# Performance work log

Measured on AMD Instinct MI355X. Metric: run time of the kernel, lower is better.

The kernel has to match this reference:

```python
import jax, jax.numpy as jnp
import numpy as np

N = 100000          # nodes per node type (paper, author)
E = 250000          # edges per relation
D_IN = 128          # input feature dim
H, C = 4, 32        # heads, channels per head (h_dim = H*C = 128)
HD = H * C
OUT = 349           # num classes
RELS = ["c", "w", "wb"]  # cites(paper->paper), writes(author->paper), written_by(paper->author)


def setup_inputs() -> dict:
    key = jax.random.key(0)
    ks = iter(jax.random.split(key, 64))
    def nrm(shape, scale=0.1):
        return jax.random.normal(next(ks), shape, jnp.float32) * scale
    inp = {
        "x_paper": jax.random.normal(next(ks), (N, D_IN), jnp.float32),
        "x_author": jax.random.normal(next(ks), (N, D_IN), jnp.float32),
        "ei_cites": jax.random.randint(next(ks), (2, E), 0, N),
        "ei_writes": jax.random.randint(next(ks), (2, E), 0, N),
        "ei_written": jax.random.randint(next(ks), (2, E), 0, N),
    }
    for l, din in [(0, D_IN), (1, HD)]:
        for r in RELS:
            inp[f"W{l}_{r}"] = nrm((din, HD))
            inp[f"as{l}_{r}"] = nrm((H, C))
            inp[f"ad{l}_{r}"] = nrm((H, C))
            inp[f"b{l}_{r}"] = jnp.zeros((HD,), jnp.float32)
    inp["lin_W"] = nrm((HD, OUT))
    inp["lin_b"] = jnp.zeros((OUT,), jnp.float32)
    return inp


def _gat_conv(x_src, x_dst, ei, W, att_s, att_d, b, n_dst):
    """PyG GATConv (concat heads, add_self_loops=False, shared lin for src/dst)."""
    h_s = (x_src @ W).reshape(-1, H, C)              # [Ns,H,C]
    h_d = (x_dst @ W).reshape(-1, H, C)              # [Nd,H,C]
    a_s = (h_s * att_s).sum(-1)                      # [Ns,H]
    a_d = (h_d * att_d).sum(-1)                      # [Nd,H]
    src, dst = ei[0], ei[1]
    e = jax.nn.leaky_relu(a_s[src] + a_d[dst], 0.2)  # [E,H]
    # segment softmax over incoming edges per dst node
    m = jax.ops.segment_max(e, dst, num_segments=n_dst)
    m = jnp.where(jnp.isfinite(m), m, 0.0)
    w = jnp.exp(e - m[dst])
    z = jax.ops.segment_sum(w, dst, num_segments=n_dst)
    alpha = w / (z[dst] + 1e-16)                     # [E,H]
    msg = h_s[src] * alpha[..., None]                # [E,H,C]
    agg = jax.ops.segment_sum(msg, dst, num_segments=n_dst)
    return agg.reshape(n_dst, HD) + b


def _forward(x_paper, x_author, ei_cites, ei_writes, ei_written, params, lin_W, lin_b):
    xp, xa = x_paper, x_author
    for l in range(2):
        p = params[l]
        # HeteroConv with sum aggregation across relations per dst node type
        op = _gat_conv(xp, xp, ei_cites, *p["c"], N) + _gat_conv(xa, xp, ei_writes, *p["w"], N)
        oa = _gat_conv(xp, xa, ei_written, *p["wb"], N)
        xp, xa = op, oa
        if l != 1:
            xp = jax.nn.leaky_relu(xp, 0.01)  # F.leaky_relu default slope
            xa = jax.nn.leaky_relu(xa, 0.01)
            # dropout: identity in eval/reference mode
    return xp @ lin_W + lin_b  # [N, OUT]


def reference(x_paper, x_author,
              W0_c, as0_c, ad0_c, b0_c, W0_w, as0_w, ad0_w, b0_w, W0_wb, as0_wb, ad0_wb, b0_wb,
              W1_c, as1_c, ad1_c, b1_c, W1_w, as1_w, ad1_w, b1_w, W1_wb, as1_wb, ad1_wb, b1_wb,
              lin_W, lin_b, ei_cites, ei_writes, ei_written):
    params = [
        {"c": (W0_c, as0_c, ad0_c, b0_c), "w": (W0_w, as0_w, ad0_w, b0_w), "wb": (W0_wb, as0_wb, ad0_wb, b0_wb)},
        {"c": (W1_c, as1_c, ad1_c, b1_c), "w": (W1_w, as1_w, ad1_w, b1_w), "wb": (W1_wb, as1_wb, ad1_wb, b1_wb)},
    ]
    return _forward(x_paper, x_author, ei_cites, ei_writes, ei_written, params, lin_W, lin_b)
```

## Files before the change

kernel.cpp:

```cpp
#include <hip/hip_runtime.h>

#define NN 100000
#define EE 250000
#define CAP 32

typedef unsigned int u32;

__global__ __launch_bounds__(256) void gemm_att(
    const float* __restrict__ X, const float* __restrict__ W,
    const float* __restrict__ atts, const float* __restrict__ attd,
    float* __restrict__ H, float* __restrict__ aS, float* __restrict__ aD)
{
    __shared__ float sW[64 * 128];
    __shared__ float sXT[128 * 32];
    const int tid = threadIdx.x;
    const size_t r0 = (size_t)blockIdx.x * 32;

    {
        int rl = tid & 31, kg = tid >> 5;
        const float4* Xr = (const float4*)(X + (r0 + rl) * 128);
#pragma unroll
        for (int t = 0; t < 4; ++t) {
            float4 u = Xr[kg * 4 + t];
            int k = kg * 16 + t * 4;
            sXT[(k + 0) * 32 + rl] = u.x;
            sXT[(k + 1) * 32 + rl] = u.y;
            sXT[(k + 2) * 32 + rl] = u.z;
            sXT[(k + 3) * 32 + rl] = u.w;
        }
    }

    const int jg = tid & 31;
    const int rg = tid >> 5;
    float acc[4][4] = {};

    for (int kh = 0; kh < 2; ++kh) {
        __syncthreads();
        const float4* Wu = (const float4*)(W + kh * 64 * 128);
        float4* sWv = (float4*)sW;
#pragma unroll
        for (int t = 0; t < 8; ++t)
            sWv[tid + 256 * t] = Wu[tid + 256 * t];
        __syncthreads();
#pragma unroll 4
        for (int k = 0; k < 64; ++k) {
            const float4 w = ((const float4*)sW)[k * 32 + jg];
            const int kk = kh * 64 + k;
            const float4 x = ((const float4*)sXT)[kk * 8 + rg];
            acc[0][0] += w.x * x.x; acc[0][1] += w.y * x.x; acc[0][2] += w.z * x.x; acc[0][3] += w.w * x.x;
            acc[1][0] += w.x * x.y; acc[1][1] += w.y * x.y; acc[1][2] += w.z * x.y; acc[1][3] += w.w * x.y;
            acc[2][0] += w.x * x.z; acc[2][1] += w.y * x.z; acc[2][2] += w.z * x.z; acc[2][3] += w.w * x.z;
            acc[3][0] += w.x * x.w; acc[3][1] += w.y * x.w; acc[3][2] += w.z * x.w; acc[3][3] += w.w * x.w;
        }
    }

    const float4 sv = ((const float4*)atts)[jg];
    const float4 dv = ((const float4*)attd)[jg];
    const int h = jg >> 3;

#pragma unroll
    for (int i = 0; i < 4; ++i) {
        const size_t row = r0 + rg * 4 + i;
        if (H)
            ((float4*)H)[row * 32 + jg] = make_float4(acc[i][0], acc[i][1], acc[i][2], acc[i][3]);
        float ps = acc[i][0] * sv.x + acc[i][1] * sv.y + acc[i][2] * sv.z + acc[i][3] * sv.w;
        float pd = acc[i][0] * dv.x + acc[i][1] * dv.y + acc[i][2] * dv.z + acc[i][3] * dv.w;
        ps += __shfl_xor(ps, 1); ps += __shfl_xor(ps, 2); ps += __shfl_xor(ps, 4);
        pd += __shfl_xor(pd, 1); pd += __shfl_xor(pd, 2); pd += __shfl_xor(pd, 4);
        if ((jg & 7) == 0) {
            aS[row * 4 + h] = ps;
            aD[row * 4 + h] = pd;
        }
    }
}

__global__ __launch_bounds__(256) void fold_w3(
    const float* __restrict__ W0, const float* __restrict__ a0,
    const float* __restrict__ W1, const float* __restrict__ a1,
    const float* __restrict__ W2, const float* __restrict__ a2,
    float* __restrict__ Wf)
{
    int i = blockIdx.x * 256 + threadIdx.x;
    if (i >= 1536) return;
    int r = i >> 9, j = i & 511;
    int k = j >> 2, h = j & 3;
    const float* W = (r == 0) ? W0 : (r == 1) ? W1 : W2;
    const float* a = (r == 0) ? a0 : (r == 1) ? a1 : a2;
    float s = 0.f;
#pragma unroll
    for (int c = 0; c < 32; ++c)
        s += W[k * 128 + h * 32 + c] * a[h * 32 + c];
    Wf[i] = s;
}

__global__ __launch_bounds__(256) void gemv_att(
    const float* __restrict__ X, const float* __restrict__ Wf,
    float* __restrict__ aD)
{
    __shared__ float sWf[512];
    const int tid = threadIdx.x;
    if (tid < 128)
        ((float4*)sWf)[tid] = ((const float4*)Wf)[tid];
    __syncthreads();
    const int t = blockIdx.x * 256 + tid;
    const int n = t >> 5, lane = t & 31;
    if (n >= NN) return;
    const float4 x = ((const float4*)X)[(size_t)n * 32 + lane];
    const float4 w0 = ((const float4*)sWf)[lane * 4 + 0];
    const float4 w1 = ((const float4*)sWf)[lane * 4 + 1];
    const float4 w2 = ((const float4*)sWf)[lane * 4 + 2];
    const float4 w3 = ((const float4*)sWf)[lane * 4 + 3];
    float p0 = x.x * w0.x + x.y * w1.x + x.z * w2.x + x.w * w3.x;
    float p1 = x.x * w0.y + x.y * w1.y + x.z * w2.y + x.w * w3.y;
    float p2 = x.x * w0.z + x.y * w1.z + x.z * w2.z + x.w * w3.z;
    float p3 = x.x * w0.w + x.y * w1.w + x.z * w2.w + x.w * w3.w;
#pragma unroll
    for (int off = 1; off < 32; off <<= 1) {
        p0 += __shfl_xor(p0, off);
        p1 += __shfl_xor(p1, off);
        p2 += __shfl_xor(p2, off);
        p3 += __shfl_xor(p3, off);
    }
    if (lane == 0)
        ((float4*)aD)[n] = make_float4(p0, p1, p2, p3);
}

__global__ __launch_bounds__(256) void fill_buckets(
    const int* __restrict__ ei, int* __restrict__ deg, int* __restrict__ bkt)
{
    int e = blockIdx.x * 256 + threadIdx.x;
    if (e >= EE) return;
    int s = ei[e], d = ei[EE + e];
    int slot = atomicAdd(&deg[d], 1);
    if (slot >= 0 && slot < CAP) bkt[(size_t)d * CAP + slot] = s;
}

__global__ __launch_bounds__(256) void aggregate(
    const int* __restrict__ deg, const int* __restrict__ bkt,
    const float* __restrict__ aS, const float* __restrict__ aD,
    const float* __restrict__ Hs, float* __restrict__ out,
    int accumulate, const float* __restrict__ b1, const float* __restrict__ b2,
    int act)
{
    int t = blockIdx.x * 256 + threadIdx.x;
    int d = t >> 5, lane = t & 31;
    if (d >= NN) return;
    int g = deg[d]; if (g > CAP) g = CAP; if (g < 0) g = 0;
    const int h = lane >> 3;
    const float adh = aD[d * 4 + h];
    const int* mybkt = bkt + (size_t)d * CAP;

    const int4 sa = *(const int4*)mybkt;
    const int4 sb = *(const int4*)(mybkt + 4);
    int sidx[8] = {sa.x, sa.y, sa.z, sa.w, sb.x, sb.y, sb.z, sb.w};
#pragma unroll
    for (int j = 0; j < 8; ++j)
        sidx[j] = (j < g) ? sidx[j] : 0;

    float e[8];
#pragma unroll
    for (int j = 0; j < 8; ++j) {
        float ev = aS[sidx[j] * 4 + h] + adh;
        e[j] = ev > 0.f ? ev : 0.2f * ev;
    }
    float m = -INFINITY;
#pragma unroll
    for (int j = 0; j < 8; ++j)
        if (j < g) m = fmaxf(m, e[j]);
    for (int j = 8; j < g; ++j) {
        int s = mybkt[j];
        float ev = aS[s * 4 + h] + adh;
        ev = ev > 0.f ? ev : 0.2f * ev;
        m = fmaxf(m, ev);
    }

    float4 acc = make_float4(0.f, 0.f, 0.f, 0.f);
    float z = 0.f;
#pragma unroll
    for (int j = 0; j < 8; ++j) {
        if (j < g) {
            float w = __expf(e[j] - m);
            z += w;
            float4 hv = ((const float4*)Hs)[(size_t)sidx[j] * 32 + lane];
            acc.x += w * hv.x; acc.y += w * hv.y; acc.z += w * hv.z; acc.w += w * hv.w;
        }
    }
    for (int j = 8; j < g; ++j) {
        int s = mybkt[j];
        float ev = aS[s * 4 + h] + adh;
        ev = ev > 0.f ? ev : 0.2f * ev;
        float w = __expf(ev - m);
        z += w;
        float4 hv = ((const float4*)Hs)[(size_t)s * 32 + lane];
        acc.x += w * hv.x; acc.y += w * hv.y; acc.z += w * hv.z; acc.w += w * hv.w;
    }
    float inv = 1.f / (z + 1e-16f);
    acc.x *= inv; acc.y *= inv; acc.z *= inv; acc.w *= inv;

    if (accumulate) {
        float4 p = ((const float4*)out)[(size_t)d * 32 + lane];
        acc.x += p.x; acc.y += p.y; acc.z += p.z; acc.w += p.w;
    }
    if (b1) {
        float4 bv = ((const float4*)b1)[lane];
        acc.x += bv.x; acc.y += bv.y; acc.z += bv.z; acc.w += bv.w;
    }
    if (b2) {
        float4 bv = ((const float4*)b2)[lane];
        acc.x += bv.x; acc.y += bv.y; acc.z += bv.z; acc.w += bv.w;
    }
    if (act) {
        acc.x = acc.x > 0.f ? acc.x : 0.01f * acc.x;
        acc.y = acc.y > 0.f ? acc.y : 0.01f * acc.y;
        acc.z = acc.z > 0.f ? acc.z : 0.01f * acc.z;
        acc.w = acc.w > 0.f ? acc.w : 0.01f * acc.w;
    }
    ((float4*)out)[(size_t)d * 32 + lane] = acc;
}

__global__ __launch_bounds__(256) void pad_w(
    const float* __restrict__ Wl, const float* __restrict__ bl,
    float* __restrict__ Wp, float* __restrict__ bp)
{
    int i = blockIdx.x * 256 + threadIdx.x;
    if (i >= 128 * 384) return;
    int k = i / 384, j = i - k * 384;
    Wp[i] = (j < 349) ? Wl[k * 349 + j] : 0.0f;
    if (i < 384) bp[i] = (i < 349) ? bl[i] : 0.0f;
}

__global__ __launch_bounds__(256) void gemm_out(
    const float* __restrict__ X, const float* __restrict__ Wp,
    const float* __restrict__ bp, float* __restrict__ out)
{
    __shared__ float sW[64 * 128];
    __shared__ float sXT[128 * 32];
    const int tid = threadIdx.x;
    const size_t r0 = (size_t)blockIdx.x * 32;

    {
        int rl = tid & 31, kg = tid >> 5;
        const float4* Xr = (const float4*)(X + (r0 + rl) * 128);
#pragma unroll
        for (int t = 0; t < 4; ++t) {
            float4 u = Xr[kg * 4 + t];
            int k = kg * 16 + t * 4;
            sXT[(k + 0) * 32 + rl] = u.x;
            sXT[(k + 1) * 32 + rl] = u.y;
            sXT[(k + 2) * 32 + rl] = u.z;
            sXT[(k + 3) * 32 + rl] = u.w;
        }
    }

    const int jg = tid & 31;
    const int rg = tid >> 5;

    for (int jt = 0; jt < 3; ++jt) {
        float acc[4][4] = {};
        for (int kh = 0; kh < 2; ++kh) {
            __syncthreads();
            {
                const float4* Wu = (const float4*)Wp;
                float4* sWv = (float4*)sW;
#pragma unroll
                for (int t = 0; t < 8; ++t) {
                    int f = tid + 256 * t;
                    int r = f >> 5, c4 = f & 31;
                    sWv[f] = Wu[(size_t)(kh * 64 + r) * 96 + jt * 32 + c4];
                }
            }
            __syncthreads();
#pragma unroll 4
            for (int k = 0; k < 64; ++k) {
                const float4 w = ((const float4*)sW)[k * 32 + jg];
                const float4 x = ((const float4*)sXT)[(kh * 64 + k) * 8 + rg];
                acc[0][0] += w.x * x.x; acc[0][1] += w.y * x.x; acc[0][2] += w.z * x.x; acc[0][3] += w.w * x.x;
                acc[1][0] += w.x * x.y; acc[1][1] += w.y * x.y; acc[1][2] += w.z * x.y; acc[1][3] += w.w * x.y;
                acc[2][0] += w.x * x.z; acc[2][1] += w.y * x.z; acc[2][2] += w.z * x.z; acc[2][3] += w.w * x.z;
                acc[3][0] += w.x * x.w; acc[3][1] += w.y * x.w; acc[3][2] += w.z * x.w; acc[3][3] += w.w * x.w;
            }
        }
        const int j = jt * 128 + jg * 4;
        const float4 bb = *(const float4*)(bp + j);
#pragma unroll
        for (int i = 0; i < 4; ++i) {
            const size_t row = r0 + rg * 4 + i;
            float* orow = out + row * 349;
            if (j + 0 < 349) orow[j + 0] = acc[i][0] + bb.x;
            if (j + 1 < 349) orow[j + 1] = acc[i][1] + bb.y;
            if (j + 2 < 349) orow[j + 2] = acc[i][2] + bb.z;
            if (j + 3 < 349) orow[j + 3] = acc[i][3] + bb.w;
        }
    }
}

extern "C" void kernel_launch(void* const* d_in, const int* in_sizes, int n_in,
                              void* d_out, int out_size, void* d_ws, size_t ws_size,
                              hipStream_t stream)
{
    (void)in_sizes; (void)n_in; (void)out_size; (void)ws_size;
    const float* xp = (const float*)d_in[0];
    const float* xa = (const float*)d_in[1];
    const int* eic = (const int*)d_in[2];
    const int* eiw = (const int*)d_in[3];
    const int* eiwb = (const int*)d_in[4];
    auto Wl = [&](int l, int r) { return (const float*)d_in[5 + (l * 3 + r) * 4 + 0]; };
    auto As = [&](int l, int r) { return (const float*)d_in[5 + (l * 3 + r) * 4 + 1]; };
    auto Ad = [&](int l, int r) { return (const float*)d_in[5 + (l * 3 + r) * 4 + 2]; };
    auto Bs = [&](int l, int r) { return (const float*)d_in[5 + (l * 3 + r) * 4 + 3]; };
    const float* linW = (const float*)d_in[29];
    const float* linb = (const float*)d_in[30];

    char* wsp = (char*)d_ws;
    auto carve = [&](size_t bytes) -> void* {
        void* p = (void*)wsp;
        wsp += (bytes + 255) & ~(size_t)255;
        return p;
    };
    float* Hs = (float*)carve((size_t)NN * 128 * 4);
    float* P1 = (float*)carve((size_t)NN * 128 * 4);
    float* A1 = (float*)carve((size_t)NN * 128 * 4);
    float* P2 = (float*)carve((size_t)NN * 128 * 4);
    int* deg = (int*)carve((size_t)NN * 3 * 4);
    int* deg_c = deg, *deg_w = deg + NN, *deg_wb = deg + 2 * NN;
    int* bkt_c = (int*)carve((size_t)NN * CAP * 4);
    int* bkt_w = (int*)carve((size_t)NN * CAP * 4);
    int* bkt_wb = (int*)carve((size_t)NN * CAP * 4);
    float* aS = (float*)carve((size_t)NN * 4 * 4);
    float* aD = (float*)carve((size_t)NN * 4 * 4);
    float* aX = (float*)carve((size_t)NN * 4 * 4);
    float* Wp = (float*)carve((size_t)128 * 384 * 4);
    float* bp = (float*)carve((size_t)384 * 4);
    float* Wf = (float*)carve((size_t)3 * 512 * 4);

    dim3 blk(256);
    const int gG = NN / 32;
    const int gE = (EE + 255) / 256;
    const int gA = NN * 32 / 256;

    hipMemsetAsync(deg, 0, (size_t)NN * 3 * 4, stream);
    fill_buckets<<<gE, blk, 0, stream>>>(eic, deg_c, bkt_c);
    fill_buckets<<<gE, blk, 0, stream>>>(eiw, deg_w, bkt_w);
    fill_buckets<<<gE, blk, 0, stream>>>(eiwb, deg_wb, bkt_wb);
    fold_w3<<<6, blk, 0, stream>>>(Wl(0, 2), Ad(0, 2), Wl(0, 1), Ad(0, 1),
                                   Wl(1, 1), Ad(1, 1), Wf);

    gemm_att<<<gG, blk, 0, stream>>>(xp, Wl(0, 2), As(0, 2), Ad(0, 2), Hs, aS, aX);
    gemv_att<<<gA, blk, 0, stream>>>(xa, Wf + 0 * 512, aD);
    aggregate<<<gA, blk, 0, stream>>>(deg_wb, bkt_wb, aS, aD, Hs, A1, 0, Bs(0, 2), nullptr, 1);

    gemm_att<<<gG, blk, 0, stream>>>(xp, Wl(0, 0), As(0, 0), Ad(0, 0), Hs, aS, aD);
    aggregate<<<gA, blk, 0, stream>>>(deg_c, bkt_c, aS, aD, Hs, P1, 0, nullptr, nullptr, 0);

    gemm_att<<<gG, blk, 0, stream>>>(xa, Wl(0, 1), As(0, 1), Ad(0, 1), Hs, aS, aX);
    gemv_att<<<gA, blk, 0, stream>>>(xp, Wf + 1 * 512, aD);
    aggregate<<<gA, blk, 0, stream>>>(deg_w, bkt_w, aS, aD, Hs, P1, 1, Bs(0, 0), Bs(0, 1), 1);

    gemm_att<<<gG, blk, 0, stream>>>(P1, Wl(1, 0), As(1, 0), Ad(1, 0), Hs, aS, aD);
    aggregate<<<gA, blk, 0, stream>>>(deg_c, bkt_c, aS, aD, Hs, P2, 0, nullptr, nullptr, 0);

    gemm_att<<<gG, blk, 0, stream>>>(A1, Wl(1, 1), As(1, 1), Ad(1, 1), Hs, aS, aX);
    gemv_att<<<gA, blk, 0, stream>>>(P1, Wf + 2 * 512, aD);
    aggregate<<<gA, blk, 0, stream>>>(deg_w, bkt_w, aS, aD, Hs, P2, 1, Bs(1, 0), Bs(1, 1), 0);

    pad_w<<<192, blk, 0, stream>>>(linW, linb, Wp, bp);
    gemm_out<<<gG, blk, 0, stream>>>(P2, Wp, bp, (float*)d_out);
}
```

Measured before the change: 959.2 us.

## Use split-bf16 MFMA for the final output projection GEMM

Rewrites the final linear layer GEMM to use bf16 MFMA instructions, splitting both activations and weights into high and low bf16 parts and summing three products to keep close to fp32 accuracy. Weights are stored transposed as bf16 hi/lo by pad_w, and activations are converted into swizzled LDS tiles of 64 rows per block. The aim is to replace the scalar fp32 FMA loop with matrix-core throughput. The cost is triple MFMA work, extra conversion arithmetic, and a small precision loss from dropping the lo*lo term.

```diff
diff --git a/kernel.cpp b/kernel.cpp
--- a/kernel.cpp
+++ b/kernel.cpp
@@ -5,6 +5,17 @@
 #define CAP 32
 
 typedef unsigned int u32;
+typedef unsigned short ushort;
+typedef __attribute__((ext_vector_type(8))) short bf16x8;
+typedef __attribute__((ext_vector_type(4))) float f32x4;
+
+__device__ __forceinline__ ushort f2bf(float x) {
+    u32 u = __float_as_uint(x);
+    return (ushort)((u + 0x7fffu + ((u >> 16) & 1u)) >> 16);
+}
+__device__ __forceinline__ float bf2f(ushort h) {
+    return __uint_as_float(((u32)h) << 16);
+}
 
 __global__ __launch_bounds__(256) void gemm_att(
     const float* __restrict__ X, const float* __restrict__ W,
@@ -220,76 +231,109 @@
 
 __global__ __launch_bounds__(256) void pad_w(
     const float* __restrict__ Wl, const float* __restrict__ bl,
-    float* __restrict__ Wp, float* __restrict__ bp)
+    ushort* __restrict__ Whi, ushort* __restrict__ Wlo, float* __restrict__ bp)
 {
     int i = blockIdx.x * 256 + threadIdx.x;
-    if (i >= 128 * 384) return;
-    int k = i / 384, j = i - k * 384;
-    Wp[i] = (j < 349) ? Wl[k * 349 + j] : 0.0f;
+    if (i >= 384 * 128) return;
+    int n = i >> 7, k = i & 127;
+    float w = (n < 349) ? Wl[k * 349 + n] : 0.0f;
+    ushort h = f2bf(w);
+    Whi[i] = h;
+    Wlo[i] = f2bf(w - bf2f(h));
     if (i < 384) bp[i] = (i < 349) ? bl[i] : 0.0f;
 }
 
 __global__ __launch_bounds__(256) void gemm_out(
-    const float* __restrict__ X, const float* __restrict__ Wp,
-    const float* __restrict__ bp, float* __restrict__ out)
-{
-    __shared__ float sW[64 * 128];
-    __shared__ float sXT[128 * 32];
+    const float* __restrict__ X, const ushort* __restrict__ Whi,
+    const ushort* __restrict__ Wlo, const float* __restrict__ bp,
+    float* __restrict__ out)
+{
+    __shared__ ushort sAhi[64 * 128];
+    __shared__ ushort sAlo[64 * 128];
     const int tid = threadIdx.x;
-    const size_t r0 = (size_t)blockIdx.x * 32;
+    const size_t r0 = (size_t)blockIdx.x * 64;
 
     {
-        int rl = tid & 31, kg = tid >> 5;
-        const float4* Xr = (const float4*)(X + (r0 + rl) * 128);
-#pragma unroll
-        for (int t = 0; t < 4; ++t) {
-            float4 u = Xr[kg * 4 + t];
-            int k = kg * 16 + t * 4;
-            sXT[(k + 0) * 32 + rl] = u.x;
-            sXT[(k + 1) * 32 + rl] = u.y;
-            sXT[(k + 2) * 32 + rl] = u.z;
-            sXT[(k + 3) * 32 + rl] = u.w;
-        }
-    }
-
-    const int jg = tid & 31;
-    const int rg = tid >> 5;
-
-    for (int jt = 0; jt < 3; ++jt) {
-        float acc[4][4] = {};
-        for (int kh = 0; kh < 2; ++kh) {
-            __syncthreads();
-            {
-                const float4* Wu = (const float4*)Wp;
-                float4* sWv = (float4*)sW;
-#pragma unroll
-                for (int t = 0; t < 8; ++t) {
-                    int f = tid + 256 * t;
-                    int r = f >> 5, c4 = f & 31;
-                    sWv[f] = Wu[(size_t)(kh * 64 + r) * 96 + jt * 32 + c4];
-                }
+        const int rl = tid >> 2, sub = tid & 3;
+        const size_t row = r0 + rl;
+        const float4* Xr = (const float4*)(X + row * 128);
+        const u32 swz = ((u32)(rl & 7)) << 4;
+        const float4 z4 = make_float4(0.f, 0.f, 0.f, 0.f);
+#pragma unroll
+        for (int i = 0; i < 4; ++i) {
+            float4 u0 = (row < NN) ? Xr[sub * 8 + 2 * i] : z4;
+            float4 u1 = (row < NN) ? Xr[sub * 8 + 2 * i + 1] : z4;
+            float v[8] = {u0.x, u0.y, u0.z, u0.w, u1.x, u1.y, u1.z, u1.w};
+            bf16x8 h8, l8;
+#pragma unroll
+            for (int e = 0; e < 8; ++e) {
+                ushort h = f2bf(v[e]);
+                h8[e] = (short)h;
+                l8[e] = (short)f2bf(v[e] - bf2f(h));
             }
-            __syncthreads();
-#pragma unroll 4
-            for (int k = 0; k < 64; ++k) {
-                const float4 w = ((const float4*)sW)[k * 32 + jg];
-                const float4 x = ((const float4*)sXT)[(kh * 64 + k) * 8 + rg];
-                acc[0][0] += w.x * x.x; acc[0][1] += w.y * x.x; acc[0][2] += w.z * x.x; acc[0][3] += w.w * x.x;
-                acc[1][0] += w.x * x.y; acc[1][1] += w.y * x.y; acc[1][2] += w.z * x.y; acc[1][3] += w.w * x.y;
-                acc[2][0] += w.x * x.z; acc[2][1] += w.y * x.z; acc[2][2] += w.z * x.z; acc[2][3] += w.w * x.z;
-                acc[3][0] += w.x * x.w; acc[3][1] += w.y * x.w; acc[3][2] += w.z * x.w; acc[3][3] += w.w * x.w;
+            u32 byteoff = ((u32)rl * 256u + (u32)((sub * 32 + i * 8) * 2)) ^ swz;
+            *(bf16x8*)((char*)sAhi + byteoff) = h8;
+            *(bf16x8*)((char*)sAlo + byteoff) = l8;
+        }
+    }
+    __syncthreads();
+
+    const int wave = tid >> 6, lane = tid & 63;
+    const int lr = lane & 15;
+    const int lg = lane >> 4;
+    const int ncol0 = wave * 96;
+
+    f32x4 acc[4][6];
+#pragma unroll
+    for (int mt = 0; mt < 4; ++mt)
+#pragma unroll
+        for (int nt = 0; nt < 6; ++nt)
+            acc[mt][nt] = (f32x4){0.f, 0.f, 0.f, 0.f};
+
+    for (int ks = 0; ks < 4; ++ks) {
+        bf16x8 ah[4], al[4];
+#pragma unroll
+        for (int mt = 0; mt < 4; ++mt) {
+            const int row = mt * 16 + lr;
+            u32 byteoff = ((u32)row * 256u + (u32)(ks * 64 + lg * 16))
+                          ^ (((u32)(row & 7)) << 4);
+            ah[mt] = *(const bf16x8*)((const char*)sAhi + byteoff);
+            al[mt] = *(const bf16x8*)((const char*)sAlo + byteoff);
+        }
+        bf16x8 bh[6], bl6[6];
+#pragma unroll
+        for (int nt = 0; nt < 6; ++nt) {
+            const int n = ncol0 + nt * 16 + lr;
+            const size_t off = (size_t)n * 128 + ks * 32 + lg * 8;
+            bh[nt]  = *(const bf16x8*)(Whi + off);
+            bl6[nt] = *(const bf16x8*)(Wlo + off);
+        }
+#pragma unroll
+        for (int mt = 0; mt < 4; ++mt)
+#pragma unroll
+            for (int nt = 0; nt < 6; ++nt) {
+                acc[mt][nt] = __builtin_amdgcn_mfma_f32_16x16x32_bf16(
+                    ah[mt], bh[nt], acc[mt][nt], 0, 0, 0);
+                acc[mt][nt] = __builtin_amdgcn_mfma_f32_16x16x32_bf16(
+                    ah[mt], bl6[nt], acc[mt][nt], 0, 0, 0);
+                acc[mt][nt] = __builtin_amdgcn_mfma_f32_16x16x32_bf16(
+                    al[mt], bh[nt], acc[mt][nt], 0, 0, 0);
             }
-        }
-        const int j = jt * 128 + jg * 4;
-        const float4 bb = *(const float4*)(bp + j);
-#pragma unroll
-        for (int i = 0; i < 4; ++i) {
-            const size_t row = r0 + rg * 4 + i;
-            float* orow = out + row * 349;
-            if (j + 0 < 349) orow[j + 0] = acc[i][0] + bb.x;
-            if (j + 1 < 349) orow[j + 1] = acc[i][1] + bb.y;
-            if (j + 2 < 349) orow[j + 2] = acc[i][2] + bb.z;
-            if (j + 3 < 349) orow[j + 3] = acc[i][3] + bb.w;
+    }
+
+#pragma unroll
+    for (int nt = 0; nt < 6; ++nt) {
+        const int n = ncol0 + nt * 16 + lr;
+        if (n >= 349) continue;
+        const float bb = bp[n];
+#pragma unroll
+        for (int mt = 0; mt < 4; ++mt) {
+#pragma unroll
+            for (int r = 0; r < 4; ++r) {
+                const size_t row = r0 + mt * 16 + lg * 4 + r;
+                if (row < NN)
+                    out[row * 349 + n] = acc[mt][nt][r] + bb;
+            }
         }
     }
 }
@@ -329,7 +373,8 @@
     float* aS = (float*)carve((size_t)NN * 4 * 4);
     float* aD = (float*)carve((size_t)NN * 4 * 4);
     float* aX = (float*)carve((size_t)NN * 4 * 4);
-    float* Wp = (float*)carve((size_t)128 * 384 * 4);
+    ushort* Whi = (ushort*)carve((size_t)384 * 128 * 2);
+    ushort* Wlo = (ushort*)carve((size_t)384 * 128 * 2);
     float* bp = (float*)carve((size_t)384 * 4);
     float* Wf = (float*)carve((size_t)3 * 512 * 4);
 
@@ -337,6 +382,7 @@
     const int gG = NN / 32;
     const int gE = (EE + 255) / 256;
     const int gA = NN * 32 / 256;
+    const int gO = (NN + 63) / 64;
 
     hipMemsetAsync(deg, 0, (size_t)NN * 3 * 4, stream);
     fill_buckets<<<gE, blk, 0, stream>>>(eic, deg_c, bkt_c);
@@ -363,6 +409,6 @@
     gemv_att<<<gA, blk, 0, stream>>>(P1, Wf + 2 * 512, aD);
     aggregate<<<gA, blk, 0, stream>>>(deg_w, bkt_w, aS, aD, Hs, P2, 1, Bs(1, 0), Bs(1, 1), 0);
 
-    pad_w<<<192, blk, 0, stream>>>(linW, linb, Wp, bp);
-    gemm_out<<<gG, blk, 0, stream>>>(P2, Wp, bp, (float*)d_out);
-}
+    pad_w<<<192, blk, 0, stream>>>(linW, linb, Whi, Wlo, bp);
+    gemm_out<<<gO, blk, 0, stream>>>(P2, Whi, Wlo, bp, (float*)d_out);
+}
```

Measured after the change: 958.0 us. No clear change (-0.1%).
